# Optimization experiments

Measured on AMD Instinct MI355X. Metric: run time of the kernel, lower is better.

## Reference

```python
import jax, jax.numpy as jnp
import numpy as np

VOCAB, EMBED, HIDDEN = 32000, 256, 64
B, T = 4096, 64


def setup_inputs() -> dict:
    key = jax.random.key(0)
    ks = jax.random.split(key, 6)
    s = 1.0 / float(np.sqrt(HIDDEN))  # PyTorch LSTM init scale
    x = jax.random.randint(ks[0], (B, T), 0, VOCAB)
    embed_table = jax.random.normal(ks[1], (VOCAB, EMBED), jnp.float32)
    W_ih = jax.random.uniform(ks[2], (4 * HIDDEN, EMBED), jnp.float32, -s, s)
    W_hh = jax.random.uniform(ks[3], (4 * HIDDEN, HIDDEN), jnp.float32, -s, s)
    b_ih = jax.random.uniform(ks[4], (4 * HIDDEN,), jnp.float32, -s, s)
    b_hh = jax.random.uniform(ks[5], (4 * HIDDEN,), jnp.float32, -s, s)
    return {"x": x, "embed_table": embed_table, "W_ih": W_ih, "W_hh": W_hh, "b_ih": b_ih, "b_hh": b_hh}


def reference(x, embed_table, W_ih, W_hh, b_ih, b_hh):
    # Embedding lookup: [B,T,E]
    emb = embed_table[x]
    # Precompute input projection for all timesteps (PyTorch gate order i,f,g,o)
    xg = jnp.einsum('bte,ge->btg', emb, W_ih) + (b_ih + b_hh)  # [B,T,4H]
    xg = jnp.swapaxes(xg, 0, 1)  # [T,B,4H]
    h0 = jnp.zeros((x.shape[0], HIDDEN), xg.dtype)
    c0 = jnp.zeros((x.shape[0], HIDDEN), xg.dtype)

    def step(carry, xt):
        h, c = carry
        g = xt + h @ W_hh.T  # [B,4H]
        i, f, gg, o = jnp.split(g, 4, axis=-1)
        c = jax.nn.sigmoid(f) * c + jax.nn.sigmoid(i) * jnp.tanh(gg)
        h = jax.nn.sigmoid(o) * jnp.tanh(c)
        return (h, c), None

    (h, _), _ = jax.lax.scan(step, (h0, c0), xg)
    return h  # [B, HIDDEN] == hidden.squeeze(0)
```

## Files before the change

kernel.cpp:

```cpp
#include <hip/hip_runtime.h>
#include <math.h>

#define B_ 4096
#define T_ 64
#define E_ 256
#define H_ 64
#define V_ 32000
#define THREADS 1024

typedef __attribute__((ext_vector_type(8))) short bf16x8;
typedef __attribute__((ext_vector_type(4))) float f32x4;
typedef __attribute__((ext_vector_type(4))) unsigned int u32x4;

__device__ __forceinline__ short f2bf(float x) {
    unsigned u = __float_as_uint(x);
    return (short)((u + 0x7FFFu + ((u >> 16) & 1u)) >> 16);
}
__device__ __forceinline__ unsigned cvt_pk_bf16(float lo, float hi) {
    unsigned r;
    asm("v_cvt_pk_bf16_f32 %0, %1, %2" : "=v"(r) : "v"(lo), "v"(hi));
    return r;
}
__device__ __forceinline__ float exp2_raw(float x) {
    float r; asm("v_exp_f32 %0, %1" : "=v"(r) : "v"(x)); return r;
}
__device__ __forceinline__ float rcp_raw(float x) {
    float r; asm("v_rcp_f32 %0, %1" : "=v"(r) : "v"(x)); return r;
}
#define LOG2E 1.442695041f

__device__ __forceinline__ void gld16(const void* g, void* l) {
    __builtin_amdgcn_global_load_lds(
        (const __attribute__((address_space(1))) void*)g,
        (__attribute__((address_space(3))) void*)l, 16, 0, 0);
}

__global__ void prep_kernel(const float* __restrict__ W_ih,
                            const float* __restrict__ W_hh,
                            const float* __restrict__ b_ih,
                            const float* __restrict__ b_hh,
                            const float* __restrict__ emb_table,
                            short* __restrict__ wih_frag,
                            short* __restrict__ whh_g,
                            float* __restrict__ bias_f,
                            short* __restrict__ emb_bf,
                            int tabN) {
    int tid = blockIdx.x * blockDim.x + threadIdx.x;
    int stride = gridDim.x * blockDim.x;
    for (int i = tid; i < 65536; i += stride) {
        int jj = i & 7;
        int l  = (i >> 3) & 63;
        int kc = (i >> 9) & 7;
        int tl = (i >> 12) & 1;
        int vv = i >> 13;
        int uu = (l & 15) >> 1, pp = l & 1;
        int g = tl * 128 + pp * 64 + vv * 8 + uu;
        int k = kc * 32 + (l >> 4) * 8 + jj;
        wih_frag[i] = f2bf(W_ih[g * E_ + k]);
    }
    for (int i = tid; i < 256 * 64; i += stride) whh_g[i] = f2bf(W_hh[i]);
    for (int i = tid; i < 256; i += stride) bias_f[i] = b_ih[i] + b_hh[i];
    for (int i = tid; i < (tabN >> 2); i += stride) {
        float4 v = ((const float4*)emb_table)[i];
        uint2 w;
        w.x = cvt_pk_bf16(v.x, v.y);
        w.y = cvt_pk_bf16(v.z, v.w);
        ((uint2*)emb_bf)[i] = w;
    }
}

template <int TAB>
__global__ __attribute__((amdgpu_flat_work_group_size(THREADS, THREADS),
                          amdgpu_waves_per_eu(4, 4)))
void lstm_f(const int* __restrict__ x,
            const float* __restrict__ embf,
            const short* __restrict__ embb,
            const short* __restrict__ wih_frag,
            const short* __restrict__ whh_g,
            const float* __restrict__ bias_f,
            float* __restrict__ out) {
    __shared__ __align__(16) short s_ef[4][4096];
    __shared__ __align__(16) short s_hf[2][1024];
    __shared__ int s_idx[1024];

    const int tid  = threadIdx.x;
    const int lane = tid & 63;
    const int wave = tid >> 6;
    const int r0   = blockIdx.x * 16;

    s_idx[(tid & 63) * 16 + (tid >> 6)] = x[(r0 + (tid >> 6)) * T_ + (tid & 63)];
    ((int*)s_hf)[tid] = 0;

    const int p  = lane & 1;
    const int c4 = lane >> 4;
    const int u  = (lane & 15) >> 1;
    const float scl2 = p ? 1.0f : 2.0f;
    const float offB = p ? 0.0f : -1.0f;
    const float enB  = -LOG2E * scl2;
    const int m0 = c4 * 4 + p * 2;

    bf16x8 wA[8], wB[8], qA0, qA1, qB0, qB1;
    float bA = 0.f, bB = 0.f;
    int hw_s = 0;
    if (wave < 8) {
        const short* wp = wih_frag + wave * 8192 + lane * 8;
        #pragma unroll
        for (int kc = 0; kc < 8; ++kc) {
            wA[kc] = *(const bf16x8*)(wp + kc * 512);
            wB[kc] = *(const bf16x8*)(wp + 4096 + kc * 512);
        }
        const int gA = p * 64 + wave * 8 + u;
        const short* qp = whh_g + gA * 64 + c4 * 8;
        qA0 = *(const bf16x8*)(qp);
        qA1 = *(const bf16x8*)(qp + 32);
        qB0 = *(const bf16x8*)(qp + 8192);
        qB1 = *(const bf16x8*)(qp + 8192 + 32);
        bA = bias_f[gA];
        bB = bias_f[gA + 128];
        hw_s = (wave >> 2) * 512 + (wave & 3) * 128
             + ((u & 1) ? (m0 + 1) * 8 + (u - 1) : m0 * 8 + u);
    }

    const int m16   = lane & 15;
    const int sbase = (wave - 8) * 512 + lane * 8;
    const int skoff = (wave - 8) * 32 + (lane >> 4) * 8;

    __syncthreads();

    if (wave >= 8) {
        #pragma unroll
        for (int tt = 0; tt < 3; ++tt) {
            int tok = s_idx[tt * 16 + m16];
            if (TAB) {
                gld16(embb + (size_t)tok * E_ + skoff,
                      &s_ef[tt][(wave - 8) * 512]);
            } else {
                const float* pr = embf + (size_t)tok * E_ + skoff;
                float4 f0 = *(const float4*)pr;
                float4 f1 = *(const float4*)(pr + 4);
                u32x4 w;
                w[0] = cvt_pk_bf16(f0.x, f0.y);
                w[1] = cvt_pk_bf16(f0.z, f0.w);
                w[2] = cvt_pk_bf16(f1.x, f1.y);
                w[3] = cvt_pk_bf16(f1.z, f1.w);
                *(u32x4*)(&s_ef[tt][0] + sbase) = w;
            }
        }
    }
    if (TAB) {
        asm volatile("s_waitcnt vmcnt(1) lgkmcnt(0)" ::: "memory");
        __builtin_amdgcn_s_barrier();
        __builtin_amdgcn_sched_barrier(0);
    } else {
        __syncthreads();
    }

    f32x4 pA, pB;
    if (wave < 8) {
        pA = (f32x4){bA, bA, bA, bA};
        pB = (f32x4){bB, bB, bB, bB};
        const short* eb = &s_ef[0][0] + lane * 8;
        #pragma unroll
        for (int kc = 0; kc < 8; ++kc) {
            bf16x8 av = *(const bf16x8*)(eb + kc * 512);
            pA = __builtin_amdgcn_mfma_f32_16x16x32_bf16(av, wA[kc], pA, 0, 0, 0);
            pB = __builtin_amdgcn_mfma_f32_16x16x32_bf16(av, wB[kc], pB, 0, 0, 0);
        }
    }

    float c0 = 0.f, c1 = 0.f, h0v = 0.f, h1v = 0.f;

    #pragma unroll 4
    for (int t = 0; t < T_; ++t) {
        if (wave < 8) {
            const short* hb = &s_hf[t & 1][0] + lane * 8;
            bf16x8 hv0 = *(const bf16x8*)(hb);
            bf16x8 hv1 = *(const bf16x8*)(hb + 512);
            __builtin_amdgcn_s_setprio(1);
            pA = __builtin_amdgcn_mfma_f32_16x16x32_bf16(hv0, qA0, pA, 0, 0, 0);
            pA = __builtin_amdgcn_mfma_f32_16x16x32_bf16(hv1, qA1, pA, 0, 0, 0);
            pB = __builtin_amdgcn_mfma_f32_16x16x32_bf16(hv0, qB0, pB, 0, 0, 0);
            pB = __builtin_amdgcn_mfma_f32_16x16x32_bf16(hv1, qB1, pB, 0, 0, 0);
            __builtin_amdgcn_s_setprio(0);

            float sA[4], Bv[4];
            #pragma unroll
            for (int q = 0; q < 4; ++q) {
                sA[q] = rcp_raw(1.0f + exp2_raw(-LOG2E * pA[q]));
                Bv[q] = rcp_raw(1.0f + exp2_raw(enB * pB[q])) * scl2 + offB;
            }
            float s1 = p ? sA[0] : sA[2] * Bv[2];
            float r1 = __shfl_xor(s1, 1);
            float s2 = p ? sA[1] : sA[3] * Bv[3];
            float r2 = __shfl_xor(s2, 1);
            float r3 = __shfl_xor(Bv[0], 1);
            float r4 = __shfl_xor(Bv[1], 1);
            float fc0 = p ? sA[2] : r1;
            float ic0 = p ? r1 : sA[0] * Bv[0];
            float oc0 = p ? Bv[2] : r3;
            float fc1 = p ? sA[3] : r2;
            float ic1 = p ? r2 : sA[1] * Bv[1];
            float oc1 = p ? Bv[3] : r4;
            c0 = fc0 * c0 + ic0;
            c1 = fc1 * c1 + ic1;
            h0v = oc0 * (1.0f - 2.0f * rcp_raw(1.0f + exp2_raw(2.0f * LOG2E * c0)));
            h1v = oc1 * (1.0f - 2.0f * rcp_raw(1.0f + exp2_raw(2.0f * LOG2E * c1)));

            float snd = (u & 1) ? h0v : h1v;
            float rcv = __shfl_xor(snd, 2);
            unsigned hw = (u & 1) ? cvt_pk_bf16(rcv, h1v) : cvt_pk_bf16(h0v, rcv);
            *(unsigned*)(&s_hf[(t + 1) & 1][0] + hw_s) = hw;

            if (t < T_ - 1) {
                pA = (f32x4){bA, bA, bA, bA};
                pB = (f32x4){bB, bB, bB, bB};
                const short* eb = &s_ef[(t + 1) & 3][0] + lane * 8;
                __builtin_amdgcn_s_setprio(1);
                #pragma unroll
                for (int kc = 0; kc < 8; ++kc) {
                    bf16x8 av = *(const bf16x8*)(eb + kc * 512);
                    pA = __builtin_amdgcn_mfma_f32_16x16x32_bf16(av, wA[kc], pA, 0, 0, 0);
                    pB = __builtin_amdgcn_mfma_f32_16x16x32_bf16(av, wB[kc], pB, 0, 0, 0);
                }
                __builtin_amdgcn_s_setprio(0);
            }
        } else {
            if (t + 3 < T_) {
                int tok = s_idx[(t + 3) * 16 + m16];
                if (TAB) {
                    gld16(embb + (size_t)tok * E_ + skoff,
                          &s_ef[(t + 3) & 3][(wave - 8) * 512]);
                } else {
                    const float* pr = embf + (size_t)tok * E_ + skoff;
                    float4 f0 = *(const float4*)pr;
                    float4 f1 = *(const float4*)(pr + 4);
                    u32x4 w;
                    w[0] = cvt_pk_bf16(f0.x, f0.y);
                    w[1] = cvt_pk_bf16(f0.z, f0.w);
                    w[2] = cvt_pk_bf16(f1.x, f1.y);
                    w[3] = cvt_pk_bf16(f1.z, f1.w);
                    *(u32x4*)(&s_ef[(t + 3) & 3][0] + sbase) = w;
                }
            }
        }
        if (TAB) {
            asm volatile("s_waitcnt vmcnt(1) lgkmcnt(0)" ::: "memory");
            __builtin_amdgcn_s_barrier();
            __builtin_amdgcn_sched_barrier(0);
        } else {
            __syncthreads();
        }
    }

    if (wave < 8) {
        const int j = wave * 8 + u;
        out[(r0 + m0) * H_ + j]     = h0v;
        out[(r0 + m0 + 1) * H_ + j] = h1v;
    }
}

extern "C" void kernel_launch(void* const* d_in, const int* in_sizes, int n_in,
                              void* d_out, int out_size, void* d_ws, size_t ws_size,
                              hipStream_t stream) {
    const int*   x         = (const int*)d_in[0];
    const float* emb_table = (const float*)d_in[1];
    const float* W_ih      = (const float*)d_in[2];
    const float* W_hh      = (const float*)d_in[3];
    const float* b_ih      = (const float*)d_in[4];
    const float* b_hh      = (const float*)d_in[5];
    float*       out       = (float*)d_out;

    short* wih_frag = (short*)d_ws;
    short* whh_g    = wih_frag + 65536;
    float* bias_f   = (float*)(whh_g + 16384);
    short* emb_bf   = (short*)(bias_f + 256);

    const size_t need = (size_t)(65536 + 16384) * 2 + 256 * 4
                      + (size_t)V_ * E_ * 2;
    const int tab = (ws_size >= need) ? 1 : 0;

    prep_kernel<<<tab ? 1024 : 64, 256, 0, stream>>>(
        W_ih, W_hh, b_ih, b_hh, emb_table,
        wih_frag, whh_g, bias_f,
        tab ? emb_bf : wih_frag, tab ? V_ * E_ : 0);

    if (tab) {
        lstm_f<1><<<B_ / 16, THREADS, 0, stream>>>(
            x, emb_table, emb_bf, wih_frag, whh_g, bias_f, out);
    } else {
        lstm_f<0><<<B_ / 16, THREADS, 0, stream>>>(
            x, emb_table, wih_frag, wih_frag, whh_g, bias_f, out);
    }
}
```

Measured before the change: 76.13 us.

## Stagger gate math across wave groups and use DPP lane swaps

```diff
diff --git a/kernel.cpp b/kernel.cpp
--- a/kernel.cpp
+++ b/kernel.cpp
@@ -28,6 +28,12 @@
     float r; asm("v_rcp_f32 %0, %1" : "=v"(r) : "v"(x)); return r;
 }
 #define LOG2E 1.442695041f
+
+template <int CTRL>
+__device__ __forceinline__ float dpp_f(float x) {
+    return __int_as_float(
+        __builtin_amdgcn_mov_dpp(__float_as_int(x), CTRL, 0xF, 0xF, true));
+}
 
 __device__ __forceinline__ void gld16(const void* g, void* l) {
     __builtin_amdgcn_global_load_lds(
@@ -81,6 +87,7 @@
             float* __restrict__ out) {
     __shared__ __align__(16) short s_ef[4][4096];
     __shared__ __align__(16) short s_hf[2][1024];
+    __shared__ __align__(16) float s_gst[4 * 512];
     __shared__ int s_idx[1024];
 
     const int tid  = threadIdx.x;
@@ -155,7 +162,10 @@
         __syncthreads();
     }
 
+    float c0 = 0.f, c1 = 0.f, h0v = 0.f, h1v = 0.f;
     f32x4 pA, pB;
+    float* sg = s_gst + (wave & 3) * 512 + lane * 8;
+
     if (wave < 8) {
         pA = (f32x4){bA, bA, bA, bA};
         pB = (f32x4){bB, bB, bB, bB};
@@ -168,7 +178,48 @@
         }
     }
 
-    float c0 = 0.f, c1 = 0.f, h0v = 0.f, h1v = 0.f;
+    auto gates_phase = [&](f32x4 GA, f32x4 GB, int t) {
+        float sA[4], Bv[4];
+        #pragma unroll
+        for (int q = 0; q < 4; ++q) {
+            sA[q] = rcp_raw(1.0f + exp2_raw(-LOG2E * GA[q]));
+            Bv[q] = rcp_raw(1.0f + exp2_raw(enB * GB[q])) * scl2 + offB;
+        }
+        float s1 = p ? sA[0] : sA[2] * Bv[2];
+        float r1 = dpp_f<0xB1>(s1);
+        float s2 = p ? sA[1] : sA[3] * Bv[3];
+        float r2 = dpp_f<0xB1>(s2);
+        float r3 = dpp_f<0xB1>(Bv[0]);
+        float r4 = dpp_f<0xB1>(Bv[1]);
+        float fc0 = p ? sA[2] : r1;
+        float ic0 = p ? r1 : sA[0] * Bv[0];
+        float oc0 = p ? Bv[2] : r3;
+        float fc1 = p ? sA[3] : r2;
+        float ic1 = p ? r2 : sA[1] * Bv[1];
+        float oc1 = p ? Bv[3] : r4;
+        c0 = fc0 * c0 + ic0;
+        c1 = fc1 * c1 + ic1;
+        h0v = oc0 * (1.0f - 2.0f * rcp_raw(1.0f + exp2_raw(2.0f * LOG2E * c0)));
+        h1v = oc1 * (1.0f - 2.0f * rcp_raw(1.0f + exp2_raw(2.0f * LOG2E * c1)));
+        float snd = (u & 1) ? h0v : h1v;
+        float rcv = dpp_f<0x4E>(snd);
+        unsigned hw = (u & 1) ? cvt_pk_bf16(rcv, h1v) : cvt_pk_bf16(h0v, rcv);
+        *(unsigned*)(&s_hf[(t + 1) & 1][0] + hw_s) = hw;
+    };
+
+    auto p_phase = [&](int t) {
+        pA = (f32x4){bA, bA, bA, bA};
+        pB = (f32x4){bB, bB, bB, bB};
+        const short* eb = &s_ef[(t + 1) & 3][0] + lane * 8;
+        __builtin_amdgcn_s_setprio(1);
+        #pragma unroll
+        for (int kc = 0; kc < 8; ++kc) {
+            bf16x8 av = *(const bf16x8*)(eb + kc * 512);
+            pA = __builtin_amdgcn_mfma_f32_16x16x32_bf16(av, wA[kc], pA, 0, 0, 0);
+            pB = __builtin_amdgcn_mfma_f32_16x16x32_bf16(av, wB[kc], pB, 0, 0, 0);
+        }
+        __builtin_amdgcn_s_setprio(0);
+    };
 
     #pragma unroll 4
     for (int t = 0; t < T_; ++t) {
@@ -183,46 +234,18 @@
             pB = __builtin_amdgcn_mfma_f32_16x16x32_bf16(hv1, qB1, pB, 0, 0, 0);
             __builtin_amdgcn_s_setprio(0);
 
-            float sA[4], Bv[4];
-            #pragma unroll
-            for (int q = 0; q < 4; ++q) {
-                sA[q] = rcp_raw(1.0f + exp2_raw(-LOG2E * pA[q]));
-                Bv[q] = rcp_raw(1.0f + exp2_raw(enB * pB[q])) * scl2 + offB;
-            }
-            float s1 = p ? sA[0] : sA[2] * Bv[2];
-            float r1 = __shfl_xor(s1, 1);
-            float s2 = p ? sA[1] : sA[3] * Bv[3];
-            float r2 = __shfl_xor(s2, 1);
-            float r3 = __shfl_xor(Bv[0], 1);
-            float r4 = __shfl_xor(Bv[1], 1);
-            float fc0 = p ? sA[2] : r1;
-            float ic0 = p ? r1 : sA[0] * Bv[0];
-            float oc0 = p ? Bv[2] : r3;
-            float fc1 = p ? sA[3] : r2;
-            float ic1 = p ? r2 : sA[1] * Bv[1];
-            float oc1 = p ? Bv[3] : r4;
-            c0 = fc0 * c0 + ic0;
-            c1 = fc1 * c1 + ic1;
-            h0v = oc0 * (1.0f - 2.0f * rcp_raw(1.0f + exp2_raw(2.0f * LOG2E * c0)));
-            h1v = oc1 * (1.0f - 2.0f * rcp_raw(1.0f + exp2_raw(2.0f * LOG2E * c1)));
-
-            float snd = (u & 1) ? h0v : h1v;
-            float rcv = __shfl_xor(snd, 2);
-            unsigned hw = (u & 1) ? cvt_pk_bf16(rcv, h1v) : cvt_pk_bf16(h0v, rcv);
-            *(unsigned*)(&s_hf[(t + 1) & 1][0] + hw_s) = hw;
-
-            if (t < T_ - 1) {
-                pA = (f32x4){bA, bA, bA, bA};
-                pB = (f32x4){bB, bB, bB, bB};
-                const short* eb = &s_ef[(t + 1) & 3][0] + lane * 8;
-                __builtin_amdgcn_s_setprio(1);
-                #pragma unroll
-                for (int kc = 0; kc < 8; ++kc) {
-                    bf16x8 av = *(const bf16x8*)(eb + kc * 512);
-                    pA = __builtin_amdgcn_mfma_f32_16x16x32_bf16(av, wA[kc], pA, 0, 0, 0);
-                    pB = __builtin_amdgcn_mfma_f32_16x16x32_bf16(av, wB[kc], pB, 0, 0, 0);
-                }
-                __builtin_amdgcn_s_setprio(0);
+            if (wave < 4) {
+                gates_phase(pA, pB, t);
+                if (t < T_ - 1) p_phase(t);
+            } else {
+                *(f32x4*)sg       = pA;
+                *(f32x4*)(sg + 4) = pB;
+                __builtin_amdgcn_sched_barrier(0);
+                if (t < T_ - 1) p_phase(t);
+                __builtin_amdgcn_sched_barrier(0);
+                f32x4 GA = *(const f32x4*)sg;
+                f32x4 GB = *(const f32x4*)(sg + 4);
+                gates_phase(GA, GB, t);
             }
         } else {
             if (t + 3 < T_) {
```

After: 66.82 us. 1.14x faster.
